# Performance work log

Hardware: AMD Instinct MI355X
Metric: run time of the kernel (lower is better)

The kernel has to match this reference:

```python
import jax, jax.numpy as jnp
import numpy as np

W_CHAMFER = 1.0
W_SMOOTH = 0.5
K_NEIGHBORS = 8


def _pairwise_sqdist(a, b):
    # a: [B,N,3], b: [B,M,3] -> [B,N,M] squared euclidean distances
    a2 = jnp.sum(a * a, axis=-1)  # [B,N]
    b2 = jnp.sum(b * b, axis=-1)  # [B,M]
    ab = jnp.einsum('bnd,bmd->bnm', a, b)  # [B,N,M]
    d2 = a2[:, :, None] + b2[:, None, :] - 2.0 * ab
    return jnp.maximum(d2, 0.0)


def _chamfer(pc1, pc2):
    d = jnp.sqrt(_pairwise_sqdist(pc1, pc2))  # [B,N,M] euclidean (matches torch.norm)
    d1 = jnp.min(d, axis=2)  # [B,N]
    d2 = jnp.min(d, axis=1)  # [B,M]
    return jnp.mean(d1) + jnp.mean(d2)


def _smoothness(pc, flow, k=K_NEIGHBORS):
    d2 = _pairwise_sqdist(pc, pc)  # [B,N,N]
    # k+1 nearest (squared dist preserves ordering); drop self (index 0)
    _, idx = jax.lax.top_k(-d2, k + 1)  # [B,N,k+1]
    idx = idx[:, :, 1:]  # [B,N,k]
    neighbor_flow = jax.vmap(lambda f, i: f[i])(flow, idx)  # [B,N,k,3]
    diff = flow[:, :, None, :] - neighbor_flow
    return jnp.mean(jnp.linalg.norm(diff, axis=-1))


def setup_inputs() -> dict:
    key = jax.random.key(0)
    k1, k2, k3 = jax.random.split(key, 3)
    B, N, M = 2, 8192, 8192
    pc1 = jax.random.normal(k1, (B, N, 3), dtype=jnp.float32)
    pc2 = jax.random.normal(k2, (B, M, 3), dtype=jnp.float32)
    pred_flow = jax.random.normal(k3, (B, N, 3), dtype=jnp.float32) * 0.1
    return {"pc1": pc1, "pc2": pc2, "pred_flow": pred_flow}


def reference(pc1, pc2, pred_flow):
    pc1_warped = pc1 + pred_flow
    l_chamfer = _chamfer(pc1_warped, pc2)
    l_smooth = _smoothness(pc1, pred_flow)
    return W_CHAMFER * l_chamfer + W_SMOOTH * l_smooth
```

## Files before the change

kernel.cpp:

```cpp
#include <hip/hip_runtime.h>

#define N_PTS 8192
#define BATCH 2
#define KNN 8
#define NSLAB 128
#define CELLS 512
#define NBLK_C 1024
#define NBLK_S 2048
#define NBLOCKS (NBLK_C + NBLK_S)

#define ARR_PC2  0
#define ARR_WARP 2
#define ARR_PC1  4
#define WS_BB0   49152
#define WS_BB1   49920
#define WS_OIDX  50688

__device__ __forceinline__ void ce(unsigned &x, unsigned &y) {
    unsigned lo = min(x, y), hi = max(x, y); x = lo; y = hi;
}

__device__ __forceinline__ void insert4(unsigned o[4], unsigned key) {
    unsigned n0 = min(o[0], key);
    unsigned n1 = max(o[0], min(o[1], key));
    unsigned n2 = max(o[1], min(o[2], key));
    unsigned n3 = max(o[2], min(o[3], key));
    o[0]=n0; o[1]=n1; o[2]=n2; o[3]=n3;
}

__device__ __forceinline__ void merge_stage8(unsigned m[8], int d) {
    unsigned p[8], c[8];
    #pragma unroll
    for (int k = 0; k < 8; ++k) p[k] = (unsigned)__shfl_xor((int)m[k], d, 64);
    #pragma unroll
    for (int k = 0; k < 8; ++k) c[k] = min(m[k], p[7-k]);
    ce(c[0],c[4]); ce(c[1],c[5]); ce(c[2],c[6]); ce(c[3],c[7]);
    ce(c[0],c[2]); ce(c[1],c[3]); ce(c[4],c[6]); ce(c[5],c[7]);
    ce(c[0],c[1]); ce(c[2],c[3]); ce(c[4],c[5]); ce(c[6],c[7]);
    #pragma unroll
    for (int k = 0; k < 8; ++k) m[k] = c[k];
}

__device__ __forceinline__ void merge64(unsigned m[8]) {
    merge_stage8(m, 1); merge_stage8(m, 2); merge_stage8(m, 4);
    merge_stage8(m, 8); merge_stage8(m, 16); merge_stage8(m, 32);
}

__device__ __forceinline__ unsigned f2o(float f) {
    unsigned u = __float_as_uint(f);
    return (u & 0x80000000u) ? ~u : (u | 0x80000000u);
}
__device__ __forceinline__ float o2f(unsigned u) {
    return __uint_as_float((u & 0x80000000u) ? (u ^ 0x80000000u) : ~u);
}

__device__ __forceinline__ unsigned spread3(unsigned v) {
    return ((v & 4u) << 4) | ((v & 2u) << 2) | (v & 1u);
}
__device__ __forceinline__ int cellof(float x, float y, float z) {
    int ix = min(7, max(0, (int)((x + 3.0f) * 1.3333333f)));
    int iy = min(7, max(0, (int)((y + 3.0f) * 1.3333333f)));
    int iz = min(7, max(0, (int)((z + 3.0f) * 1.3333333f)));
    return (int)((spread3((unsigned)ix) << 2) | (spread3((unsigned)iy) << 1)
                 | spread3((unsigned)iz));
}

__device__ __forceinline__ float boxd2(const float4 bn, const float4 bx,
                                       float x, float y, float z) {
    float tx = fmaxf(fmaxf(bn.x - x, x - bx.x), 0.0f);
    float ty = fmaxf(fmaxf(bn.y - y, y - bx.y), 0.0f);
    float tz = fmaxf(fmaxf(bn.z - z, z - bx.z), 0.0f);
    return fmaf(tx, tx, fmaf(ty, ty, tz * tz));
}

__global__ __launch_bounds__(512) void pack_sort_kernel(
        const float* __restrict__ pc1, const float* __restrict__ pc2,
        const float* __restrict__ flow, float4* __restrict__ ws,
        unsigned* __restrict__ oidx) {
    __shared__ unsigned hist[CELLS];
    __shared__ unsigned offs[CELLS];
    __shared__ unsigned bbn[NSLAB * 3], bbx[NSLAB * 3];
    const int arr = blockIdx.x, t = threadIdx.x;
    const int bbatch = arr & 1;
    const bool warped = (arr >= 2 && arr < 4);
    const float* A = (arr < 2) ? pc2 : pc1;
    const size_t base = (size_t)bbatch * N_PTS * 3;

    for (int i = t; i < CELLS; i += 512) hist[i] = 0u;
    for (int i = t; i < NSLAB * 3; i += 512) { bbn[i] = 0xFFFFFFFFu; bbx[i] = 0u; }
    __syncthreads();

    int cid[16];
    #pragma unroll
    for (int k = 0; k < 16; ++k) {
        int i = t * 16 + k;
        float x = A[base + i*3+0], y = A[base + i*3+1], z = A[base + i*3+2];
        if (warped) { x += flow[base+i*3+0]; y += flow[base+i*3+1]; z += flow[base+i*3+2]; }
        cid[k] = cellof(x, y, z);
        atomicAdd(&hist[cid[k]], 1u);
    }
    __syncthreads();

    if (t < 64) {
        unsigned loc[8], s = 0;
        #pragma unroll
        for (int q = 0; q < 8; ++q) { loc[q] = s; s += hist[t*8 + q]; }
        unsigned run = s;
        #pragma unroll
        for (int d = 1; d < 64; d <<= 1) {
            unsigned v = (unsigned)__shfl_up((int)run, d, 64);
            if (t >= d) run += v;
        }
        unsigned bse = run - s;
        #pragma unroll
        for (int q = 0; q < 8; ++q) offs[t*8 + q] = bse + loc[q];
    }
    __syncthreads();

    #pragma unroll
    for (int k = 0; k < 16; ++k) {
        int i = t * 16 + k;
        float x = A[base + i*3+0], y = A[base + i*3+1], z = A[base + i*3+2];
        if (warped) { x += flow[base+i*3+0]; y += flow[base+i*3+1]; z += flow[base+i*3+2]; }
        unsigned pos = atomicAdd(&offs[cid[k]], 1u);
        ws[(size_t)arr * N_PTS + pos] = make_float4(x, y, z, fmaf(x, x, fmaf(y, y, z*z)));
        if (arr >= 4) oidx[(size_t)(arr - 4) * N_PTS + pos] = (unsigned)i;
        int s = (int)(pos >> 6);
        atomicMin(&bbn[s*3+0], f2o(x)); atomicMax(&bbx[s*3+0], f2o(x));
        atomicMin(&bbn[s*3+1], f2o(y)); atomicMax(&bbx[s*3+1], f2o(y));
        atomicMin(&bbn[s*3+2], f2o(z)); atomicMax(&bbx[s*3+2], f2o(z));
    }
    __syncthreads();

    for (int s = t; s < NSLAB; s += 512) {
        ws[WS_BB0 + (size_t)arr * NSLAB + s] =
            make_float4(o2f(bbn[s*3+0]), o2f(bbn[s*3+1]), o2f(bbn[s*3+2]), 0.0f);
        ws[WS_BB1 + (size_t)arr * NSLAB + s] =
            make_float4(o2f(bbx[s*3+0]), o2f(bbx[s*3+1]), o2f(bbx[s*3+2]), 0.0f);
    }
}

__global__ __launch_bounds__(256, 4) void mega_kernel(
        const float4* __restrict__ ws, const float* __restrict__ flow,
        const unsigned* __restrict__ oidx, float* __restrict__ out) {
    __shared__ float psum[4];
    const int tid = threadIdx.x, bx = blockIdx.x;
    const int lane = tid & 63, wv = tid >> 6;
    const int ri = bx / 3, role = bx % 3;

    if (role == 2) {
        const int z = ri >> 8, bb = z & 1, dir = z >> 1;
        const int cb = ri & 255;
        const int ca = (dir == 0 ? ARR_PC2 : ARR_WARP) + bb;
        const int ra = (dir == 0 ? ARR_WARP : ARR_PC2) + bb;
        const float4* rows = ws + (size_t)ra * N_PTS;
        const float4* cand = ws + (size_t)ca * N_PTS;
        const float4* bmn = ws + WS_BB0 + (size_t)ca * NSLAB;
        const float4* bmx = ws + WS_BB1 + (size_t)ca * NSLAB;
        const int rbase = cb * 32 + wv * 8;

        float rx[8], ry[8], rz[8], bmin[8];
        #pragma unroll
        for (int k = 0; k < 8; ++k) {
            float4 q = rows[rbase + k];
            rx[k] = q.x; ry[k] = q.y; rz[k] = q.z;
            bmin[k] = __builtin_inff();
        }
        float4 bn0 = bmn[lane], bx0 = bmx[lane];
        float4 bn1 = bmn[lane + 64], bx1 = bmx[lane + 64];
        float lb0[8], lb1[8];
        unsigned long long sm0 = 0ull, sm1 = 0ull;
        #pragma unroll
        for (int k = 0; k < 8; ++k) {
            lb0[k] = boxd2(bn0, bx0, rx[k], ry[k], rz[k]);
            lb1[k] = boxd2(bn1, bx1, rx[k], ry[k], rz[k]);
            unsigned k0 = (__float_as_uint(lb0[k]) & 0xFFFFFF80u) | (unsigned)lane;
            unsigned k1 = (__float_as_uint(lb1[k]) & 0xFFFFFF80u) | (unsigned)(lane + 64);
            unsigned kk = min(k0, k1);
            #pragma unroll
            for (int d = 1; d < 64; d <<= 1)
                kk = min(kk, (unsigned)__shfl_xor((int)kk, d, 64));
            unsigned s = kk & 127u;
            if (s < 64) sm0 |= 1ull << s; else sm1 |= 1ull << (s - 64);
        }
        auto scan_slab = [&](int s) {
            float4 c = cand[s * 64 + lane];
            #pragma unroll
            for (int k = 0; k < 8; ++k) {
                float dx = rx[k] - c.x, dy = ry[k] - c.y, dz = rz[k] - c.z;
                bmin[k] = fminf(bmin[k], fmaf(dx, dx, fmaf(dy, dy, dz * dz)));
            }
        };
        { unsigned long long m = sm0; while (m) { int s = __ffsll((unsigned long long)m) - 1; m &= m - 1; scan_slab(s); } }
        { unsigned long long m = sm1; while (m) { int s = __ffsll((unsigned long long)m) - 1; m &= m - 1; scan_slab(s + 64); } }
        bool p0 = false, p1 = false;
        #pragma unroll
        for (int k = 0; k < 8; ++k) {
            float u = bmin[k];
            #pragma unroll
            for (int d = 1; d < 64; d <<= 1)
                u = fminf(u, __shfl_xor(u, d, 64));
            p0 |= (lb0[k] < u);
            p1 |= (lb1[k] < u);
        }
        unsigned long long q0 = __ballot(p0) & ~sm0;
        unsigned long long q1 = __ballot(p1) & ~sm1;
        while (q0) { int s = __ffsll(q0) - 1; q0 &= q0 - 1; scan_slab(s); }
        while (q1) { int s = __ffsll(q1) - 1; q1 &= q1 - 1; scan_slab(s + 64); }
        #pragma unroll
        for (int k = 0; k < 8; ++k) {
            #pragma unroll
            for (int d = 1; d < 64; d <<= 1)
                bmin[k] = fminf(bmin[k], __shfl_xor(bmin[k], d, 64));
        }
        if (lane == 0) {
            float val = 0.0f;
            #pragma unroll
            for (int k = 0; k < 8; ++k) val += sqrtf(fmaxf(bmin[k], 0.0f));
            psum[wv] = val;
        }
        __syncthreads();
        if (tid == 0) {
            float ch = psum[0] + psum[1] + psum[2] + psum[3];
            atomicAdd(out, ch * (1.0f / (float)(BATCH * N_PTS)));
        }
    } else {
        const int sbx = ri * 2 + role;
        const int b = sbx >> 10, sx = sbx & 1023;
        const int i0w = sx * 8 + wv * 2;
        const float4* cand = ws + (size_t)(ARR_PC1 + b) * N_PTS;
        const float4* bmn = ws + WS_BB0 + (size_t)(ARR_PC1 + b) * NSLAB;
        const float4* bmx = ws + WS_BB1 + (size_t)(ARR_PC1 + b) * NSLAB;
        const unsigned* OI = oidx + (size_t)b * N_PTS;
        const float* F = flow + (size_t)b * N_PTS * 3;

        float rx[2], ry[2], rz[2], thrf[2];
        unsigned thr[2], o[2][4];
        #pragma unroll
        for (int r = 0; r < 2; ++r) {
            float4 q = cand[i0w + r];
            rx[r] = q.x; ry[r] = q.y; rz[r] = q.z;
            thr[r] = 0xFFFFFFFFu;
            #pragma unroll
            for (int k = 0; k < 4; ++k) o[r][k] = 0xFFFFFFFFu;
        }
        float4 bn0 = bmn[lane], bx0 = bmx[lane];
        float4 bn1 = bmn[lane + 64], bx1 = bmx[lane + 64];
        float lb0[2], lb1[2];
        unsigned long long sm0 = 0ull, sm1 = 0ull;
        { int so = i0w >> 6;
          if (so < 64) sm0 |= 1ull << so; else sm1 |= 1ull << (so - 64); }
        #pragma unroll
        for (int r = 0; r < 2; ++r) {
            lb0[r] = boxd2(bn0, bx0, rx[r], ry[r], rz[r]);
            lb1[r] = boxd2(bn1, bx1, rx[r], ry[r], rz[r]);
            unsigned k0 = (__float_as_uint(lb0[r]) & 0xFFFFFF80u) | (unsigned)lane;
            unsigned k1 = (__float_as_uint(lb1[r]) & 0xFFFFFF80u) | (unsigned)(lane + 64);
            unsigned kk = min(k0, k1);
            #pragma unroll
            for (int d = 1; d < 64; d <<= 1)
                kk = min(kk, (unsigned)__shfl_xor((int)kk, d, 64));
            unsigned s = kk & 127u;
            if (s < 64) sm0 |= 1ull << s; else sm1 |= 1ull << (s - 64);
        }
        auto scan_slab = [&](int s) {
            float4 c = cand[s * 64 + lane];
            int j = s * 64 + lane;
            #pragma unroll
            for (int r = 0; r < 2; ++r) {
                float dx = rx[r] - c.x, dy = ry[r] - c.y, dz = rz[r] - c.z;
                float d2 = fmaf(dx, dx, fmaf(dy, dy, dz * dz));
                unsigned key = (__float_as_uint(d2) & 0xFFFFE000u) | (unsigned)j;
                key = (j == i0w + r) ? 0xFFFFFFFFu : key;
                insert4(o[r], key);
            }
        };
        { unsigned long long m = sm0; while (m) { int s = __ffsll(m) - 1; m &= m - 1; scan_slab(s); } }
        { unsigned long long m = sm1; while (m) { int s = __ffsll(m) - 1; m &= m - 1; scan_slab(s + 64); } }
        #pragma unroll
        for (int r = 0; r < 2; ++r) {
            unsigned m0 = o[r][0], m1 = o[r][1], m2 = o[r][2], m3 = o[r][3];
            #pragma unroll
            for (int d = 1; d <= 16; d <<= 1) {
                unsigned q0 = (unsigned)__shfl_xor((int)m0, d, 64);
                unsigned q1 = (unsigned)__shfl_xor((int)m1, d, 64);
                unsigned q2 = (unsigned)__shfl_xor((int)m2, d, 64);
                unsigned q3 = (unsigned)__shfl_xor((int)m3, d, 64);
                unsigned c0 = min(m0, q3), c1 = min(m1, q2);
                unsigned c2 = min(m2, q1), c3 = min(m3, q0);
                ce(c0, c2); ce(c1, c3); ce(c0, c1); ce(c2, c3);
                m0 = c0; m1 = c1; m2 = c2; m3 = c3;
            }
            unsigned bound = max(m3, (unsigned)__shfl_xor((int)m3, 32, 64));
            thr[r] = min(thr[r], bound);
            thrf[r] = __uint_as_float((thr[r] & 0xFFFFE000u) + 0x4000u);
        }
        bool p0 = (lb0[0] < thrf[0]) | (lb0[1] < thrf[1]);
        bool p1 = (lb1[0] < thrf[0]) | (lb1[1] < thrf[1]);
        unsigned long long q0 = __ballot(p0) & ~sm0;
        unsigned long long q1 = __ballot(p1) & ~sm1;
        while (q0) { int s = __ffsll(q0) - 1; q0 &= q0 - 1; scan_slab(s); }
        while (q1) { int s = __ffsll(q1) - 1; q1 &= q1 - 1; scan_slab(s + 64); }

        const int sel = lane & 15;
        const int pr = sel >> 3, kk = sel & 7;
        unsigned mykey = 0xFFFFFFFFu;
        #pragma unroll
        for (int r = 0; r < 2; ++r) {
            unsigned m[8] = {o[r][0], o[r][1], o[r][2], o[r][3],
                             0xFFFFFFFFu, 0xFFFFFFFFu, 0xFFFFFFFFu, 0xFFFFFFFFu};
            merge64(m);
            if (pr == r) {
                unsigned k2 = m[0];
                #pragma unroll
                for (int t2 = 1; t2 < 8; ++t2) k2 = (kk == t2) ? m[t2] : k2;
                mykey = k2;
            }
        }
        const int isrt = i0w + pr;
        const int io = (int)OI[isrt];
        const int j  = (int)(mykey & (N_PTS - 1));
        const int jo = (int)OI[j];
        float dx = F[io*3+0] - F[jo*3+0];
        float dy = F[io*3+1] - F[jo*3+1];
        float dz = F[io*3+2] - F[jo*3+2];
        float sv = sqrtf(fmaf(dx, dx, fmaf(dy, dy, dz * dz)));
        #pragma unroll
        for (int d = 1; d < 64; d <<= 1) sv += __shfl_xor(sv, d, 64);
        if (lane == 0) psum[wv] = sv;
        __syncthreads();

        if (tid == 0) {
            float sm = psum[0] + psum[1] + psum[2] + psum[3];
            atomicAdd(out, sm * (0.125f / ((float)BATCH * N_PTS * KNN)));
        }
    }
}

extern "C" void kernel_launch(void* const* d_in, const int* in_sizes, int n_in,
                              void* d_out, int out_size, void* d_ws, size_t ws_size,
                              hipStream_t stream) {
    const float* pc1  = (const float*)d_in[0];
    const float* pc2  = (const float*)d_in[1];
    const float* flow = (const float*)d_in[2];
    float* out = (float*)d_out;
    float4* ws4 = (float4*)d_ws;
    unsigned* oidx = (unsigned*)(ws4 + WS_OIDX);

    pack_sort_kernel<<<dim3(6), 512, 0, stream>>>(pc1, pc2, flow, ws4, oidx);
    mega_kernel<<<dim3(NBLOCKS), 256, 0, stream>>>(ws4, flow, oidx, out);
}
```

Before: 167.8 us.

## Use persistent per-wave work stealing with centroid seed slab and prefetched slab scans

Replaces static block-to-work mapping with a persistent kernel in which each wave grabs units from a global atomic counter, with units scrambled by a multiplicative permutation to balance the chamfer and kNN work. The chamfer path now seeds from the one slab nearest the row group's centroid instead of each row's nearest slab. The kNN path seeds only from its own slab. Slab loads are software-prefetched one ahead of use, and block-level shared sync per unit is replaced by shared atomic accumulation. This aims to remove load imbalance and tail effects, at the cost of global atomics, weaker initial pruning bounds that may force more slab scans, and reliance on the counter reset in the first kernel.

```diff
diff --git a/kernel.cpp b/kernel.cpp
--- a/kernel.cpp
+++ b/kernel.cpp
@@ -5,9 +5,10 @@
 #define KNN 8
 #define NSLAB 128
 #define CELLS 512
-#define NBLK_C 1024
-#define NBLK_S 2048
-#define NBLOCKS (NBLK_C + NBLK_S)
+#define NUNIT_C 4096
+#define NUNIT_S 8192
+#define NUNITS  (NUNIT_C + NUNIT_S)
+#define NBLOCKS 2048
 
 #define ARR_PC2  0
 #define ARR_WARP 2
@@ -15,6 +16,7 @@
 #define WS_BB0   49152
 #define WS_BB1   49920
 #define WS_OIDX  50688
+#define WS_CTR   54784
 
 __device__ __forceinline__ void ce(unsigned &x, unsigned &y) {
     unsigned lo = min(x, y), hi = max(x, y); x = lo; y = hi;
@@ -73,10 +75,16 @@
     return fmaf(tx, tx, fmaf(ty, ty, tz * tz));
 }
 
+__device__ __forceinline__ int popslab(unsigned long long &m0, unsigned long long &m1) {
+    if (m0) { int s = __ffsll(m0) - 1; m0 &= m0 - 1; return s; }
+    if (m1) { int s = __ffsll(m1) - 1; m1 &= m1 - 1; return s + 64; }
+    return -1;
+}
+
 __global__ __launch_bounds__(512) void pack_sort_kernel(
         const float* __restrict__ pc1, const float* __restrict__ pc2,
         const float* __restrict__ flow, float4* __restrict__ ws,
-        unsigned* __restrict__ oidx) {
+        unsigned* __restrict__ oidx, unsigned* __restrict__ ctr) {
     __shared__ unsigned hist[CELLS];
     __shared__ unsigned offs[CELLS];
     __shared__ unsigned bbn[NSLAB * 3], bbx[NSLAB * 3];
@@ -85,6 +93,8 @@
     const bool warped = (arr >= 2 && arr < 4);
     const float* A = (arr < 2) ? pc2 : pc1;
     const size_t base = (size_t)bbatch * N_PTS * 3;
+
+    if (arr == 0 && t == 0) ctr[0] = 0u;
 
     for (int i = t; i < CELLS; i += 512) hist[i] = 0u;
     for (int i = t; i < NSLAB * 3; i += 512) { bbn[i] = 0xFFFFFFFFu; bbx[i] = 0u; }
@@ -142,199 +152,221 @@
 
 __global__ __launch_bounds__(256, 4) void mega_kernel(
         const float4* __restrict__ ws, const float* __restrict__ flow,
-        const unsigned* __restrict__ oidx, float* __restrict__ out) {
-    __shared__ float psum[4];
-    const int tid = threadIdx.x, bx = blockIdx.x;
-    const int lane = tid & 63, wv = tid >> 6;
-    const int ri = bx / 3, role = bx % 3;
-
-    if (role == 2) {
-        const int z = ri >> 8, bb = z & 1, dir = z >> 1;
-        const int cb = ri & 255;
-        const int ca = (dir == 0 ? ARR_PC2 : ARR_WARP) + bb;
-        const int ra = (dir == 0 ? ARR_WARP : ARR_PC2) + bb;
-        const float4* rows = ws + (size_t)ra * N_PTS;
-        const float4* cand = ws + (size_t)ca * N_PTS;
-        const float4* bmn = ws + WS_BB0 + (size_t)ca * NSLAB;
-        const float4* bmx = ws + WS_BB1 + (size_t)ca * NSLAB;
-        const int rbase = cb * 32 + wv * 8;
-
-        float rx[8], ry[8], rz[8], bmin[8];
-        #pragma unroll
-        for (int k = 0; k < 8; ++k) {
-            float4 q = rows[rbase + k];
-            rx[k] = q.x; ry[k] = q.y; rz[k] = q.z;
-            bmin[k] = __builtin_inff();
-        }
-        float4 bn0 = bmn[lane], bx0 = bmx[lane];
-        float4 bn1 = bmn[lane + 64], bx1 = bmx[lane + 64];
-        float lb0[8], lb1[8];
-        unsigned long long sm0 = 0ull, sm1 = 0ull;
-        #pragma unroll
-        for (int k = 0; k < 8; ++k) {
-            lb0[k] = boxd2(bn0, bx0, rx[k], ry[k], rz[k]);
-            lb1[k] = boxd2(bn1, bx1, rx[k], ry[k], rz[k]);
-            unsigned k0 = (__float_as_uint(lb0[k]) & 0xFFFFFF80u) | (unsigned)lane;
-            unsigned k1 = (__float_as_uint(lb1[k]) & 0xFFFFFF80u) | (unsigned)(lane + 64);
-            unsigned kk = min(k0, k1);
+        const unsigned* __restrict__ oidx, unsigned* __restrict__ ctr,
+        float* __restrict__ out) {
+    __shared__ float bacc;
+    const int tid = threadIdx.x;
+    const int lane = tid & 63;
+    if (tid == 0) bacc = 0.0f;
+    __syncthreads();
+
+    for (;;) {
+        unsigned got = 0;
+        if (lane == 0) got = atomicAdd(ctr, 1u);
+        got = (unsigned)__shfl((int)got, 0, 64);
+        if (got >= NUNITS) break;
+        const unsigned up = (got * 2749u) % (unsigned)NUNITS;
+
+        if (up < NUNIT_C) {
+            const int z = (int)(up >> 10), bb = z & 1, dir = z >> 1;
+            const int rbase = (int)(up & 1023) * 8;
+            const int ca = (dir == 0 ? ARR_PC2 : ARR_WARP) + bb;
+            const int ra = (dir == 0 ? ARR_WARP : ARR_PC2) + bb;
+            const float4* rows = ws + (size_t)ra * N_PTS;
+            const float4* cand = ws + (size_t)ca * N_PTS;
+            const float4* bmn = ws + WS_BB0 + (size_t)ca * NSLAB;
+            const float4* bmx = ws + WS_BB1 + (size_t)ca * NSLAB;
+
+            float rx[8], ry[8], rz[8], bmin[8];
+            float cx = 0.f, cy = 0.f, cz = 0.f;
+            #pragma unroll
+            for (int k = 0; k < 8; ++k) {
+                float4 q = rows[rbase + k];
+                rx[k] = q.x; ry[k] = q.y; rz[k] = q.z;
+                cx += q.x; cy += q.y; cz += q.z;
+                bmin[k] = __builtin_inff();
+            }
+            cx *= 0.125f; cy *= 0.125f; cz *= 0.125f;
+
+            float4 bn0 = bmn[lane], bx0 = bmx[lane];
+            float4 bn1 = bmn[lane + 64], bx1 = bmx[lane + 64];
+            float lb0[8], lb1[8];
+            #pragma unroll
+            for (int k = 0; k < 8; ++k) {
+                lb0[k] = boxd2(bn0, bx0, rx[k], ry[k], rz[k]);
+                lb1[k] = boxd2(bn1, bx1, rx[k], ry[k], rz[k]);
+            }
+            float cl0 = boxd2(bn0, bx0, cx, cy, cz);
+            float cl1 = boxd2(bn1, bx1, cx, cy, cz);
+            unsigned kk = min((__float_as_uint(cl0) & 0xFFFFFF80u) | (unsigned)lane,
+                              (__float_as_uint(cl1) & 0xFFFFFF80u) | (unsigned)(lane + 64));
             #pragma unroll
             for (int d = 1; d < 64; d <<= 1)
                 kk = min(kk, (unsigned)__shfl_xor((int)kk, d, 64));
-            unsigned s = kk & 127u;
-            if (s < 64) sm0 |= 1ull << s; else sm1 |= 1ull << (s - 64);
+            const int sseed = (int)(kk & 127u);
+            {
+                float4 c = cand[sseed * 64 + lane];
+                #pragma unroll
+                for (int k = 0; k < 8; ++k) {
+                    float dx = rx[k]-c.x, dy = ry[k]-c.y, dz = rz[k]-c.z;
+                    bmin[k] = fminf(bmin[k], fmaf(dx, dx, fmaf(dy, dy, dz*dz)));
+                }
+            }
+            #pragma unroll
+            for (int k = 0; k < 8; ++k) {
+                #pragma unroll
+                for (int d = 1; d < 64; d <<= 1)
+                    bmin[k] = fminf(bmin[k], __shfl_xor(bmin[k], d, 64));
+            }
+            bool p0 = false, p1 = false;
+            #pragma unroll
+            for (int k = 0; k < 8; ++k) { p0 |= (lb0[k] < bmin[k]); p1 |= (lb1[k] < bmin[k]); }
+            unsigned long long q0 = __ballot(p0), q1 = __ballot(p1);
+            if (sseed < 64) q0 &= ~(1ull << sseed); else q1 &= ~(1ull << (sseed - 64));
+
+            int s = popslab(q0, q1);
+            if (s >= 0) {
+                float4 c = cand[s * 64 + lane];
+                for (;;) {
+                    int sn = popslab(q0, q1);
+                    float4 cn;
+                    if (sn >= 0) cn = cand[sn * 64 + lane];
+                    #pragma unroll
+                    for (int k = 0; k < 8; ++k) {
+                        float dx = rx[k]-c.x, dy = ry[k]-c.y, dz = rz[k]-c.z;
+                        bmin[k] = fminf(bmin[k], fmaf(dx, dx, fmaf(dy, dy, dz*dz)));
+                    }
+                    if (sn < 0) break;
+                    c = cn;
+                }
+            }
+            #pragma unroll
+            for (int k = 0; k < 8; ++k) {
+                #pragma unroll
+                for (int d = 1; d < 64; d <<= 1)
+                    bmin[k] = fminf(bmin[k], __shfl_xor(bmin[k], d, 64));
+            }
+            if (lane == 0) {
+                float val = 0.0f;
+                #pragma unroll
+                for (int k = 0; k < 8; ++k) val += sqrtf(fmaxf(bmin[k], 0.0f));
+                atomicAdd(&bacc, val * (1.0f / (float)(BATCH * N_PTS)));
+            }
+        } else {
+            const int su = (int)(up - NUNIT_C);
+            const int b = su >> 12;
+            const int i0w = (su & 4095) * 2;
+            const float4* cand = ws + (size_t)(ARR_PC1 + b) * N_PTS;
+            const float4* bmn = ws + WS_BB0 + (size_t)(ARR_PC1 + b) * NSLAB;
+            const float4* bmx = ws + WS_BB1 + (size_t)(ARR_PC1 + b) * NSLAB;
+            const unsigned* OI = oidx + (size_t)b * N_PTS;
+            const float* F = flow + (size_t)b * N_PTS * 3;
+
+            float rx[2], ry[2], rz[2], thrf[2];
+            unsigned o[2][4];
+            #pragma unroll
+            for (int r = 0; r < 2; ++r) {
+                float4 q = cand[i0w + r];
+                rx[r] = q.x; ry[r] = q.y; rz[r] = q.z;
+                #pragma unroll
+                for (int k = 0; k < 4; ++k) o[r][k] = 0xFFFFFFFFu;
+            }
+            float4 bn0 = bmn[lane], bx0 = bmx[lane];
+            float4 bn1 = bmn[lane + 64], bx1 = bmx[lane + 64];
+            float lb0[2], lb1[2];
+            #pragma unroll
+            for (int r = 0; r < 2; ++r) {
+                lb0[r] = boxd2(bn0, bx0, rx[r], ry[r], rz[r]);
+                lb1[r] = boxd2(bn1, bx1, rx[r], ry[r], rz[r]);
+            }
+            const int sown = i0w >> 6;
+            {
+                float4 c = cand[sown * 64 + lane];
+                int j = sown * 64 + lane;
+                #pragma unroll
+                for (int r = 0; r < 2; ++r) {
+                    float dx = rx[r]-c.x, dy = ry[r]-c.y, dz = rz[r]-c.z;
+                    float d2 = fmaf(dx, dx, fmaf(dy, dy, dz*dz));
+                    unsigned key = (__float_as_uint(d2) & 0xFFFFE000u) | (unsigned)j;
+                    key = (j == i0w + r) ? 0xFFFFFFFFu : key;
+                    insert4(o[r], key);
+                }
+            }
+            #pragma unroll
+            for (int r = 0; r < 2; ++r) {
+                unsigned m0 = o[r][0], m1 = o[r][1], m2 = o[r][2], m3 = o[r][3];
+                #pragma unroll
+                for (int d = 1; d <= 16; d <<= 1) {
+                    unsigned a0 = (unsigned)__shfl_xor((int)m0, d, 64);
+                    unsigned a1 = (unsigned)__shfl_xor((int)m1, d, 64);
+                    unsigned a2 = (unsigned)__shfl_xor((int)m2, d, 64);
+                    unsigned a3 = (unsigned)__shfl_xor((int)m3, d, 64);
+                    unsigned c0 = min(m0, a3), c1 = min(m1, a2);
+                    unsigned c2 = min(m2, a1), c3 = min(m3, a0);
+                    ce(c0, c2); ce(c1, c3); ce(c0, c1); ce(c2, c3);
+                    m0 = c0; m1 = c1; m2 = c2; m3 = c3;
+                }
+                unsigned bound = max(m3, (unsigned)__shfl_xor((int)m3, 32, 64));
+                thrf[r] = __uint_as_float((bound & 0xFFFFE000u) + 0x4000u);
+            }
+            bool p0 = (lb0[0] < thrf[0]) | (lb0[1] < thrf[1]);
+            bool p1 = (lb1[0] < thrf[0]) | (lb1[1] < thrf[1]);
+            unsigned long long q0 = __ballot(p0), q1 = __ballot(p1);
+            if (sown < 64) q0 &= ~(1ull << sown); else q1 &= ~(1ull << (sown - 64));
+
+            int s = popslab(q0, q1);
+            if (s >= 0) {
+                float4 c = cand[s * 64 + lane];
+                int j = s * 64 + lane;
+                for (;;) {
+                    int sn = popslab(q0, q1);
+                    float4 cn; int jn = 0;
+                    if (sn >= 0) { cn = cand[sn * 64 + lane]; jn = sn * 64 + lane; }
+                    #pragma unroll
+                    for (int r = 0; r < 2; ++r) {
+                        float dx = rx[r]-c.x, dy = ry[r]-c.y, dz = rz[r]-c.z;
+                        float d2 = fmaf(dx, dx, fmaf(dy, dy, dz*dz));
+                        unsigned key = (__float_as_uint(d2) & 0xFFFFE000u) | (unsigned)j;
+                        key = (j == i0w + r) ? 0xFFFFFFFFu : key;
+                        insert4(o[r], key);
+                    }
+                    if (sn < 0) break;
+                    c = cn; j = jn;
+                }
+            }
+
+            const int sel = lane & 15;
+            const int pr = sel >> 3, kq = sel & 7;
+            unsigned mykey = 0xFFFFFFFFu;
+            #pragma unroll
+            for (int r = 0; r < 2; ++r) {
+                unsigned m[8] = {o[r][0], o[r][1], o[r][2], o[r][3],
+                                 0xFFFFFFFFu, 0xFFFFFFFFu, 0xFFFFFFFFu, 0xFFFFFFFFu};
+                merge64(m);
+                if (pr == r) {
+                    unsigned k2 = m[0];
+                    #pragma unroll
+                    for (int t2 = 1; t2 < 8; ++t2) k2 = (kq == t2) ? m[t2] : k2;
+                    mykey = k2;
+                }
+            }
+            const int isrt = i0w + pr;
+            const int io = (int)OI[isrt];
+            const int j  = (int)(mykey & (N_PTS - 1));
+            const int jo = (int)OI[j];
+            float dx = F[io*3+0] - F[jo*3+0];
+            float dy = F[io*3+1] - F[jo*3+1];
+            float dz = F[io*3+2] - F[jo*3+2];
+            float sv = sqrtf(fmaf(dx, dx, fmaf(dy, dy, dz * dz)));
+            #pragma unroll
+            for (int d = 1; d < 64; d <<= 1) sv += __shfl_xor(sv, d, 64);
+            if (lane == 0)
+                atomicAdd(&bacc, sv * (0.125f / ((float)BATCH * N_PTS * KNN)));
         }
-        auto scan_slab = [&](int s) {
-            float4 c = cand[s * 64 + lane];
-            #pragma unroll
-            for (int k = 0; k < 8; ++k) {
-                float dx = rx[k] - c.x, dy = ry[k] - c.y, dz = rz[k] - c.z;
-                bmin[k] = fminf(bmin[k], fmaf(dx, dx, fmaf(dy, dy, dz * dz)));
-            }
-        };
-        { unsigned long long m = sm0; while (m) { int s = __ffsll((unsigned long long)m) - 1; m &= m - 1; scan_slab(s); } }
-        { unsigned long long m = sm1; while (m) { int s = __ffsll((unsigned long long)m) - 1; m &= m - 1; scan_slab(s + 64); } }
-        bool p0 = false, p1 = false;
-        #pragma unroll
-        for (int k = 0; k < 8; ++k) {
-            float u = bmin[k];
-            #pragma unroll
-            for (int d = 1; d < 64; d <<= 1)
-                u = fminf(u, __shfl_xor(u, d, 64));
-            p0 |= (lb0[k] < u);
-            p1 |= (lb1[k] < u);
-        }
-        unsigned long long q0 = __ballot(p0) & ~sm0;
-        unsigned long long q1 = __ballot(p1) & ~sm1;
-        while (q0) { int s = __ffsll(q0) - 1; q0 &= q0 - 1; scan_slab(s); }
-        while (q1) { int s = __ffsll(q1) - 1; q1 &= q1 - 1; scan_slab(s + 64); }
-        #pragma unroll
-        for (int k = 0; k < 8; ++k) {
-            #pragma unroll
-            for (int d = 1; d < 64; d <<= 1)
-                bmin[k] = fminf(bmin[k], __shfl_xor(bmin[k], d, 64));
-        }
-        if (lane == 0) {
-            float val = 0.0f;
-            #pragma unroll
-            for (int k = 0; k < 8; ++k) val += sqrtf(fmaxf(bmin[k], 0.0f));
-            psum[wv] = val;
-        }
-        __syncthreads();
-        if (tid == 0) {
-            float ch = psum[0] + psum[1] + psum[2] + psum[3];
-            atomicAdd(out, ch * (1.0f / (float)(BATCH * N_PTS)));
-        }
-    } else {
-        const int sbx = ri * 2 + role;
-        const int b = sbx >> 10, sx = sbx & 1023;
-        const int i0w = sx * 8 + wv * 2;
-        const float4* cand = ws + (size_t)(ARR_PC1 + b) * N_PTS;
-        const float4* bmn = ws + WS_BB0 + (size_t)(ARR_PC1 + b) * NSLAB;
-        const float4* bmx = ws + WS_BB1 + (size_t)(ARR_PC1 + b) * NSLAB;
-        const unsigned* OI = oidx + (size_t)b * N_PTS;
-        const float* F = flow + (size_t)b * N_PTS * 3;
-
-        float rx[2], ry[2], rz[2], thrf[2];
-        unsigned thr[2], o[2][4];
-        #pragma unroll
-        for (int r = 0; r < 2; ++r) {
-            float4 q = cand[i0w + r];
-            rx[r] = q.x; ry[r] = q.y; rz[r] = q.z;
-            thr[r] = 0xFFFFFFFFu;
-            #pragma unroll
-            for (int k = 0; k < 4; ++k) o[r][k] = 0xFFFFFFFFu;
-        }
-        float4 bn0 = bmn[lane], bx0 = bmx[lane];
-        float4 bn1 = bmn[lane + 64], bx1 = bmx[lane + 64];
-        float lb0[2], lb1[2];
-        unsigned long long sm0 = 0ull, sm1 = 0ull;
-        { int so = i0w >> 6;
-          if (so < 64) sm0 |= 1ull << so; else sm1 |= 1ull << (so - 64); }
-        #pragma unroll
-        for (int r = 0; r < 2; ++r) {
-            lb0[r] = boxd2(bn0, bx0, rx[r], ry[r], rz[r]);
-            lb1[r] = boxd2(bn1, bx1, rx[r], ry[r], rz[r]);
-            unsigned k0 = (__float_as_uint(lb0[r]) & 0xFFFFFF80u) | (unsigned)lane;
-            unsigned k1 = (__float_as_uint(lb1[r]) & 0xFFFFFF80u) | (unsigned)(lane + 64);
-            unsigned kk = min(k0, k1);
-            #pragma unroll
-            for (int d = 1; d < 64; d <<= 1)
-                kk = min(kk, (unsigned)__shfl_xor((int)kk, d, 64));
-            unsigned s = kk & 127u;
-            if (s < 64) sm0 |= 1ull << s; else sm1 |= 1ull << (s - 64);
-        }
-        auto scan_slab = [&](int s) {
-            float4 c = cand[s * 64 + lane];
-            int j = s * 64 + lane;
-            #pragma unroll
-            for (int r = 0; r < 2; ++r) {
-                float dx = rx[r] - c.x, dy = ry[r] - c.y, dz = rz[r] - c.z;
-                float d2 = fmaf(dx, dx, fmaf(dy, dy, dz * dz));
-                unsigned key = (__float_as_uint(d2) & 0xFFFFE000u) | (unsigned)j;
-                key = (j == i0w + r) ? 0xFFFFFFFFu : key;
-                insert4(o[r], key);
-            }
-        };
-        { unsigned long long m = sm0; while (m) { int s = __ffsll(m) - 1; m &= m - 1; scan_slab(s); } }
-        { unsigned long long m = sm1; while (m) { int s = __ffsll(m) - 1; m &= m - 1; scan_slab(s + 64); } }
-        #pragma unroll
-        for (int r = 0; r < 2; ++r) {
-            unsigned m0 = o[r][0], m1 = o[r][1], m2 = o[r][2], m3 = o[r][3];
-            #pragma unroll
-            for (int d = 1; d <= 16; d <<= 1) {
-                unsigned q0 = (unsigned)__shfl_xor((int)m0, d, 64);
-                unsigned q1 = (unsigned)__shfl_xor((int)m1, d, 64);
-                unsigned q2 = (unsigned)__shfl_xor((int)m2, d, 64);
-                unsigned q3 = (unsigned)__shfl_xor((int)m3, d, 64);
-                unsigned c0 = min(m0, q3), c1 = min(m1, q2);
-                unsigned c2 = min(m2, q1), c3 = min(m3, q0);
-                ce(c0, c2); ce(c1, c3); ce(c0, c1); ce(c2, c3);
-                m0 = c0; m1 = c1; m2 = c2; m3 = c3;
-            }
-            unsigned bound = max(m3, (unsigned)__shfl_xor((int)m3, 32, 64));
-            thr[r] = min(thr[r], bound);
-            thrf[r] = __uint_as_float((thr[r] & 0xFFFFE000u) + 0x4000u);
-        }
-        bool p0 = (lb0[0] < thrf[0]) | (lb0[1] < thrf[1]);
-        bool p1 = (lb1[0] < thrf[0]) | (lb1[1] < thrf[1]);
-        unsigned long long q0 = __ballot(p0) & ~sm0;
-        unsigned long long q1 = __ballot(p1) & ~sm1;
-        while (q0) { int s = __ffsll(q0) - 1; q0 &= q0 - 1; scan_slab(s); }
-        while (q1) { int s = __ffsll(q1) - 1; q1 &= q1 - 1; scan_slab(s + 64); }
-
-        const int sel = lane & 15;
-        const int pr = sel >> 3, kk = sel & 7;
-        unsigned mykey = 0xFFFFFFFFu;
-        #pragma unroll
-        for (int r = 0; r < 2; ++r) {
-            unsigned m[8] = {o[r][0], o[r][1], o[r][2], o[r][3],
-                             0xFFFFFFFFu, 0xFFFFFFFFu, 0xFFFFFFFFu, 0xFFFFFFFFu};
-            merge64(m);
-            if (pr == r) {
-                unsigned k2 = m[0];
-                #pragma unroll
-                for (int t2 = 1; t2 < 8; ++t2) k2 = (kk == t2) ? m[t2] : k2;
-                mykey = k2;
-            }
-        }
-        const int isrt = i0w + pr;
-        const int io = (int)OI[isrt];
-        const int j  = (int)(mykey & (N_PTS - 1));
-        const int jo = (int)OI[j];
-        float dx = F[io*3+0] - F[jo*3+0];
-        float dy = F[io*3+1] - F[jo*3+1];
-        float dz = F[io*3+2] - F[jo*3+2];
-        float sv = sqrtf(fmaf(dx, dx, fmaf(dy, dy, dz * dz)));
-        #pragma unroll
-        for (int d = 1; d < 64; d <<= 1) sv += __shfl_xor(sv, d, 64);
-        if (lane == 0) psum[wv] = sv;
-        __syncthreads();
-
-        if (tid == 0) {
-            float sm = psum[0] + psum[1] + psum[2] + psum[3];
-            atomicAdd(out, sm * (0.125f / ((float)BATCH * N_PTS * KNN)));
-        }
-    }
+    }
+
+    __syncthreads();
+    if (tid == 0) atomicAdd(out, bacc);
 }
 
 extern "C" void kernel_launch(void* const* d_in, const int* in_sizes, int n_in,
@@ -346,7 +378,8 @@
     float* out = (float*)d_out;
     float4* ws4 = (float4*)d_ws;
     unsigned* oidx = (unsigned*)(ws4 + WS_OIDX);
-
-    pack_sort_kernel<<<dim3(6), 512, 0, stream>>>(pc1, pc2, flow, ws4, oidx);
-    mega_kernel<<<dim3(NBLOCKS), 256, 0, stream>>>(ws4, flow, oidx, out);
-}
+    unsigned* ctr  = (unsigned*)(ws4 + WS_CTR);
+
+    pack_sort_kernel<<<dim3(6), 512, 0, stream>>>(pc1, pc2, flow, ws4, oidx, ctr);
+    mega_kernel<<<dim3(NBLOCKS), 256, 0, stream>>>(ws4, flow, oidx, ctr, out);
+}
```

New measurement: 342.7 us. 2.04x slower.
